# Performance work log

Hardware: AMD Instinct MI355X
Metric: run time of the kernel (lower is better)

The kernel has to match this reference:

```python
import jax, jax.numpy as jnp
import numpy as np

N_NODES = 100000


def _degrees(idx, n):
    d = jax.ops.segment_sum(jnp.ones(idx.shape[0], jnp.float32), idx, num_segments=n)
    return jnp.maximum(d, 1.0)  # DGL clamps zero degrees to 1


def graph_conv(src, dst, x, W, b, n):
    # DGL GraphConv with norm='both': out = D_in^{-1/2} A D_out^{-1/2} x W + b
    norm_src = _degrees(src, n) ** -0.5  # out-degree of source nodes
    norm_dst = _degrees(dst, n) ** -0.5  # in-degree of destination nodes
    xs = x * norm_src[:, None]
    msgs = xs[src]                                    # [E, d] gather
    agg = jax.ops.segment_sum(msgs, dst, num_segments=n)  # [N, d] scatter-add
    agg = agg * norm_dst[:, None]
    return agg @ W + b


def setup_inputs() -> dict:
    key = jax.random.key(0)
    k = jax.random.split(key, 7)
    E = 1600000
    in_f, h_f, out_f = 128, 128, 64
    return {
        "in_feat": jax.random.normal(k[0], (N_NODES, in_f), jnp.float32),
        "src": jax.random.randint(k[1], (E,), 0, N_NODES, jnp.int32),
        "dst": jax.random.randint(k[2], (E,), 0, N_NODES, jnp.int32),
        "W1": jax.random.normal(k[3], (in_f, h_f), jnp.float32) * (1.0 / np.sqrt(in_f)),
        "b1": jnp.zeros((h_f,), jnp.float32),
        "W2": jax.random.normal(k[4], (h_f, out_f), jnp.float32) * (1.0 / np.sqrt(h_f)),
        "b2": jnp.zeros((out_f,), jnp.float32),
    }


def reference(in_feat, src, dst, W1, b1, W2, b2):
    h = graph_conv(src, dst, in_feat, W1, b1, N_NODES)
    h = jax.nn.relu(h)
    h = graph_conv(src, dst, h, W2, b2, N_NODES)
    return h
```

## Files before the change

kernel.cpp:

```cpp
#include <hip/hip_runtime.h>

#define SLOT_CAP 64
#define NB_MAX 1024
#define CAP 2560

typedef __attribute__((ext_vector_type(8))) short bf16x8;
typedef __attribute__((ext_vector_type(4))) float f32x4;

__device__ __forceinline__ unsigned int bf16_rne(float f) {
    unsigned int u = __float_as_uint(f);
    return (u + 0x7FFFu + ((u >> 16) & 1u)) >> 16;
}
__device__ __forceinline__ unsigned int pack2(float a, float b) {
    return bf16_rne(a) | (bf16_rne(b) << 16);
}
__device__ __forceinline__ float bflo(unsigned int u) { return __uint_as_float(u << 16); }
__device__ __forceinline__ float bfhi(unsigned int u) { return __uint_as_float(u & 0xFFFF0000u); }
__device__ __forceinline__ float bf16val(unsigned int h) { return __uint_as_float(h << 16); }

__device__ __forceinline__ void gemm_tile(
    unsigned short* smem_us,
    const float* __restrict__ A,
    const unsigned short* __restrict__ wt_hi_g, const unsigned short* __restrict__ wt_lo_g,
    unsigned short* __restrict__ C, int M, int row0, int tid)
{
    unsigned short* As_hi = smem_us;
    unsigned short* As_lo = As_hi + 64 * 40;
    unsigned short* Ws_hi = As_lo + 64 * 40;
    unsigned short* Ws_lo = Ws_hi + 128 * 40;

    const int wv = tid >> 6;
    const int ln = tid & 63;
    const int fr = ln & 15;
    const int fk = ln >> 4;

    f32x4 acc[8];
#pragma unroll
    for (int t = 0; t < 8; t++) acc[t] = (f32x4){0.0f, 0.0f, 0.0f, 0.0f};

    const int sr = tid >> 2;
    const int sq = (tid & 3) * 8;

    for (int k0 = 0; k0 < 128; k0 += 32) {
        __syncthreads();
        {
            const int row = row0 + sr;
            float v0 = 0, v1 = 0, v2 = 0, v3 = 0, v4 = 0, v5 = 0, v6 = 0, v7 = 0;
            if (row < M) {
                const float4 p0 = *(const float4*)&A[(size_t)row * 128 + k0 + sq];
                const float4 p1 = *(const float4*)&A[(size_t)row * 128 + k0 + sq + 4];
                v0 = p0.x; v1 = p0.y; v2 = p0.z; v3 = p0.w;
                v4 = p1.x; v5 = p1.y; v6 = p1.z; v7 = p1.w;
            }
            unsigned int h0 = bf16_rne(v0), h1 = bf16_rne(v1), h2 = bf16_rne(v2), h3 = bf16_rne(v3);
            unsigned int h4 = bf16_rne(v4), h5 = bf16_rne(v5), h6 = bf16_rne(v6), h7 = bf16_rne(v7);
            uint4 hi, lo;
            hi.x = h0 | (h1 << 16); hi.y = h2 | (h3 << 16);
            hi.z = h4 | (h5 << 16); hi.w = h6 | (h7 << 16);
            lo.x = bf16_rne(v0 - bf16val(h0)) | (bf16_rne(v1 - bf16val(h1)) << 16);
            lo.y = bf16_rne(v2 - bf16val(h2)) | (bf16_rne(v3 - bf16val(h3)) << 16);
            lo.z = bf16_rne(v4 - bf16val(h4)) | (bf16_rne(v5 - bf16val(h5)) << 16);
            lo.w = bf16_rne(v6 - bf16val(h6)) | (bf16_rne(v7 - bf16val(h7)) << 16);
            *(uint4*)&As_hi[sr * 40 + sq] = hi;
            *(uint4*)&As_lo[sr * 40 + sq] = lo;
        }
#pragma unroll
        for (int j = 0; j < 8; j++) {
            int idx = tid + 256 * j;
            int c = idx >> 4, k2 = (idx & 15) * 2;
            *(unsigned int*)&Ws_hi[c * 40 + k2] = *(const unsigned int*)&wt_hi_g[c * 128 + k0 + k2];
            *(unsigned int*)&Ws_lo[c * 40 + k2] = *(const unsigned int*)&wt_lo_g[c * 128 + k0 + k2];
        }
        __syncthreads();

        bf16x8 ah = *(const bf16x8*)&As_hi[(16 * wv + fr) * 40 + fk * 8];
        bf16x8 al = *(const bf16x8*)&As_lo[(16 * wv + fr) * 40 + fk * 8];
#pragma unroll
        for (int t = 0; t < 8; t++) {
            bf16x8 bh = *(const bf16x8*)&Ws_hi[(16 * t + fr) * 40 + fk * 8];
            bf16x8 bl = *(const bf16x8*)&Ws_lo[(16 * t + fr) * 40 + fk * 8];
            acc[t] = __builtin_amdgcn_mfma_f32_16x16x32_bf16(ah, bh, acc[t], 0, 0, 0);
            acc[t] = __builtin_amdgcn_mfma_f32_16x16x32_bf16(al, bh, acc[t], 0, 0, 0);
            acc[t] = __builtin_amdgcn_mfma_f32_16x16x32_bf16(ah, bl, acc[t], 0, 0, 0);
        }
    }
#pragma unroll
    for (int t = 0; t < 8; t++) {
#pragma unroll
        for (int rg = 0; rg < 4; rg++) {
            int row = row0 + 16 * wv + fk * 4 + rg;
            if (row < M) C[(size_t)row * 128 + 16 * t + fr] = (unsigned short)bf16_rne(acc[t][rg]);
        }
    }
}

__global__ __launch_bounds__(256) void prep_w_kernel(
    const float* __restrict__ W1, unsigned short* __restrict__ wt_hi,
    unsigned short* __restrict__ wt_lo, int* __restrict__ cursor, int NB)
{
    if (blockIdx.x >= 64) {
        for (int i = (blockIdx.x - 64) * 256 + threadIdx.x; i < 2 * NB; i += 512)
            cursor[i] = 0;
        return;
    }
    const int idx = blockIdx.x * 256 + threadIdx.x;
    const int c = idx >> 7, k = idx & 127;
    float v = W1[k * 128 + c];
    unsigned int h = bf16_rne(v);
    wt_hi[idx] = (unsigned short)h;
    wt_lo[idx] = (unsigned short)bf16_rne(v - bf16val(h));
}

__global__ __launch_bounds__(256) void kb_kernel(
    const int* __restrict__ src, const int* __restrict__ dst,
    int* __restrict__ cursor,
    unsigned int* __restrict__ edge_shuf,
    unsigned char* __restrict__ src_shuf,
    int E, int NB, int EB,
    const float* __restrict__ A,
    const unsigned short* __restrict__ wt_hi_g, const unsigned short* __restrict__ wt_lo_g,
    unsigned short* __restrict__ C, int M)
{
    __shared__ __align__(16) char smem_raw[30720];
    const int tid = threadIdx.x;
    const int bid = blockIdx.x;

    if (bid >= EB) {
        int row0 = (bid - EB) * 64;
        if (row0 < M) gemm_tile((unsigned short*)smem_raw, A, wt_hi_g, wt_lo_g, C, M, row0, tid);
        return;
    }

    int* cntL = (int*)smem_raw;
    int* ofsL = cntL + 2 * NB_MAX;
    const int base = bid * 8192;
    for (int b = tid; b < 2 * NB; b += 256) cntL[b] = 0;
    __syncthreads();
#pragma unroll
    for (int it = 0; it < 8; it++) {
        const int i4 = base + (it * 256 + tid) * 4;
        if (i4 + 3 < E) {
            int4 s = *(const int4*)(src + i4);
            int4 d = *(const int4*)(dst + i4);
            atomicAdd(&cntL[d.x >> 7], 1); atomicAdd(&cntL[d.y >> 7], 1);
            atomicAdd(&cntL[d.z >> 7], 1); atomicAdd(&cntL[d.w >> 7], 1);
            atomicAdd(&cntL[NB + (s.x >> 7)], 1); atomicAdd(&cntL[NB + (s.y >> 7)], 1);
            atomicAdd(&cntL[NB + (s.z >> 7)], 1); atomicAdd(&cntL[NB + (s.w >> 7)], 1);
        } else {
            for (int i = i4; i < E && i < i4 + 4; i++) {
                atomicAdd(&cntL[dst[i] >> 7], 1);
                atomicAdd(&cntL[NB + (src[i] >> 7)], 1);
            }
        }
    }
    __syncthreads();
    for (int b = tid; b < 2 * NB; b += 256) {
        int c = cntL[b];
        ofsL[b] = c ? atomicAdd(&cursor[b], c) : 0;
    }
    __syncthreads();
#pragma unroll
    for (int it = 0; it < 8; it++) {
        const int i4 = base + (it * 256 + tid) * 4;
        if (i4 + 3 < E) {
            int4 s = *(const int4*)(src + i4);
            int4 d = *(const int4*)(dst + i4);
            { int bb = d.x >> 7; int p = atomicAdd(&ofsL[bb], 1); if (p < CAP) edge_shuf[(size_t)bb * CAP + p] = (unsigned)s.x | ((unsigned)(d.x & 127) << 17); }
            { int bb = d.y >> 7; int p = atomicAdd(&ofsL[bb], 1); if (p < CAP) edge_shuf[(size_t)bb * CAP + p] = (unsigned)s.y | ((unsigned)(d.y & 127) << 17); }
            { int bb = d.z >> 7; int p = atomicAdd(&ofsL[bb], 1); if (p < CAP) edge_shuf[(size_t)bb * CAP + p] = (unsigned)s.z | ((unsigned)(d.z & 127) << 17); }
            { int bb = d.w >> 7; int p = atomicAdd(&ofsL[bb], 1); if (p < CAP) edge_shuf[(size_t)bb * CAP + p] = (unsigned)s.w | ((unsigned)(d.w & 127) << 17); }
            { int bb = s.x >> 7; int q = atomicAdd(&ofsL[NB + bb], 1); if (q < CAP) src_shuf[(size_t)bb * CAP + q] = (unsigned char)(s.x & 127); }
            { int bb = s.y >> 7; int q = atomicAdd(&ofsL[NB + bb], 1); if (q < CAP) src_shuf[(size_t)bb * CAP + q] = (unsigned char)(s.y & 127); }
            { int bb = s.z >> 7; int q = atomicAdd(&ofsL[NB + bb], 1); if (q < CAP) src_shuf[(size_t)bb * CAP + q] = (unsigned char)(s.z & 127); }
            { int bb = s.w >> 7; int q = atomicAdd(&ofsL[NB + bb], 1); if (q < CAP) src_shuf[(size_t)bb * CAP + q] = (unsigned char)(s.w & 127); }
        } else {
            for (int i = i4; i < E && i < i4 + 4; i++) {
                int sv = src[i], dv = dst[i];
                int bb = dv >> 7; int p = atomicAdd(&ofsL[bb], 1);
                if (p < CAP) edge_shuf[(size_t)bb * CAP + p] = (unsigned)sv | ((unsigned)(dv & 127) << 17);
                int bs = sv >> 7; int q = atomicAdd(&ofsL[NB + bs], 1);
                if (q < CAP) src_shuf[(size_t)bs * CAP + q] = (unsigned char)(sv & 127);
            }
        }
    }
}

__global__ __launch_bounds__(256) void kc_src_kernel(
    const unsigned char* __restrict__ src_shuf, const int* __restrict__ cursor,
    int* __restrict__ cnt_src, int N, int NB)
{
    __shared__ int cntL[128];
    const int tid = threadIdx.x;
    const int b = blockIdx.x;
    if (tid < 128) cntL[tid] = 0;
    __syncthreads();
    const int start = b * CAP;
    const int len = min(cursor[NB + b], CAP);
    for (int i = start + tid; i < start + len; i += 256)
        atomicAdd(&cntL[src_shuf[i]], 1);
    __syncthreads();
    if (tid < 128) {
        int node = b * 128 + tid;
        if (node < N) cnt_src[node] = cntL[tid];
    }
}

#define ACC8(V_, S_) \
    acc[0] = fmaf(bflo((V_).x), (S_), acc[0]); acc[1] = fmaf(bfhi((V_).x), (S_), acc[1]); \
    acc[2] = fmaf(bflo((V_).y), (S_), acc[2]); acc[3] = fmaf(bfhi((V_).y), (S_), acc[3]); \
    acc[4] = fmaf(bflo((V_).z), (S_), acc[4]); acc[5] = fmaf(bfhi((V_).z), (S_), acc[5]); \
    acc[6] = fmaf(bflo((V_).w), (S_), acc[6]); acc[7] = fmaf(bfhi((V_).w), (S_), acc[7]);

#define SUM8(V_) \
    acc[0] += bflo((V_).x); acc[1] += bfhi((V_).x); \
    acc[2] += bflo((V_).y); acc[3] += bfhi((V_).y); \
    acc[4] += bflo((V_).z); acc[5] += bfhi((V_).z); \
    acc[6] += bflo((V_).w); acc[7] += bfhi((V_).w);

__global__ __launch_bounds__(256) void pg2_kernel(
    const int* __restrict__ cnt_src, const unsigned int* __restrict__ edge_shuf,
    const int* __restrict__ cursor,
    const unsigned int* __restrict__ msg,
    const float* __restrict__ W2, const float* __restrict__ b1,
    unsigned short* __restrict__ C, int N)
{
    __shared__ int cntL[32];
    __shared__ __align__(16) unsigned int slotsW[32 * SLOT_CAP];
    __shared__ unsigned int Agp[64][66];
    const int tid = threadIdx.x;
    const int hb = blockIdx.x;
    const int m0 = hb * 64;
    const int lane = tid & 15;
    const int b = hb >> 1;
    const int start = b * CAP;
    const int len = min(cursor[b], CAP);

#pragma unroll
    for (int half = 0; half < 2; half++) {
        if (tid < 32) cntL[tid] = 0;
        __syncthreads();
        const int dlo = (hb & 1) * 64 + half * 32;
        for (int i = start + tid; i < start + len; i += 256) {
            unsigned e = edge_shuf[i];
            int d = (int)(e >> 17) - dlo;
            if ((unsigned)d < 32u) {
                unsigned s = e & 0x1FFFFu;
                unsigned deg = (unsigned)min(cnt_src[s], 255);
                int r = atomicAdd(&cntL[d], 1);
                if (r < SLOT_CAP) slotsW[d * SLOT_CAP + r] = s | (deg << 17);
            }
        }
        __syncthreads();
#pragma unroll
        for (int p = 0; p < 2; p++) {
            const int nl32 = p * 16 + (tid >> 4);
            const int nl = half * 32 + nl32;
            const int node = m0 + nl;
            float acc[8];
#pragma unroll
            for (int k = 0; k < 8; k++) acc[k] = 0.0f;
            if (node < N) {
                const unsigned int* sl = &slotsW[nl32 * SLOT_CAP];
                const int cd = cntL[nl32];
                const int len2 = min(cd, SLOT_CAP);
                int j = 0;
                for (; j + 7 < len2; j += 8) {
                    uint4 e0 = *(const uint4*)(sl + j);
                    uint4 e1 = *(const uint4*)(sl + j + 4);
                    uint4 a0 = *(const uint4*)(msg + (size_t)(e0.x & 0x1FFFFu) * 64 + lane * 4);
                    uint4 a1 = *(const uint4*)(msg + (size_t)(e0.y & 0x1FFFFu) * 64 + lane * 4);
                    uint4 a2 = *(const uint4*)(msg + (size_t)(e0.z & 0x1FFFFu) * 64 + lane * 4);
                    uint4 a3 = *(const uint4*)(msg + (size_t)(e0.w & 0x1FFFFu) * 64 + lane * 4);
                    uint4 a4 = *(const uint4*)(msg + (size_t)(e1.x & 0x1FFFFu) * 64 + lane * 4);
                    uint4 a5 = *(const uint4*)(msg + (size_t)(e1.y & 0x1FFFFu) * 64 + lane * 4);
                    uint4 a6 = *(const uint4*)(msg + (size_t)(e1.z & 0x1FFFFu) * 64 + lane * 4);
                    uint4 a7 = *(const uint4*)(msg + (size_t)(e1.w & 0x1FFFFu) * 64 + lane * 4);
                    float w0 = rsqrtf((float)(e0.x >> 17));
                    float w1 = rsqrtf((float)(e0.y >> 17));
                    float w2 = rsqrtf((float)(e0.z >> 17));
                    float w3 = rsqrtf((float)(e0.w >> 17));
                    float w4 = rsqrtf((float)(e1.x >> 17));
                    float w5 = rsqrtf((float)(e1.y >> 17));
                    float w6 = rsqrtf((float)(e1.z >> 17));
                    float w7 = rsqrtf((float)(e1.w >> 17));
                    ACC8(a0, w0) ACC8(a1, w1) ACC8(a2, w2) ACC8(a3, w3)
                    ACC8(a4, w4) ACC8(a5, w5) ACC8(a6, w6) ACC8(a7, w7)
                }
                for (; j + 3 < len2; j += 4) {
                    uint4 e0 = *(const uint4*)(sl + j);
                    uint4 a0 = *(const uint4*)(msg + (size_t)(e0.x & 0x1FFFFu) * 64 + lane * 4);
                    uint4 a1 = *(const uint4*)(msg + (size_t)(e0.y & 0x1FFFFu) * 64 + lane * 4);
                    uint4 a2 = *(const uint4*)(msg + (size_t)(e0.z & 0x1FFFFu) * 64 + lane * 4);
                    uint4 a3 = *(const uint4*)(msg + (size_t)(e0.w & 0x1FFFFu) * 64 + lane * 4);
                    float w0 = rsqrtf((float)(e0.x >> 17));
                    float w1 = rsqrtf((float)(e0.y >> 17));
                    float w2 = rsqrtf((float)(e0.z >> 17));
                    float w3 = rsqrtf((float)(e0.w >> 17));
                    ACC8(a0, w0) ACC8(a1, w1) ACC8(a2, w2) ACC8(a3, w3)
                }
                for (; j < len2; j++) {
                    unsigned e = sl[j];
                    uint4 a0 = *(const uint4*)(msg + (size_t)(e & 0x1FFFFu) * 64 + lane * 4);
                    float w0 = rsqrtf((float)(e >> 17));
                    ACC8(a0, w0)
                }
                float nd = rsqrtf(fmaxf((float)cd, 1.0f));
                float ns = rsqrtf(fmaxf((float)cnt_src[node], 1.0f));
                float4 bA = *(const float4*)(b1 + lane * 8);
                float4 bB = *(const float4*)(b1 + lane * 8 + 4);
                acc[0] = fmaxf(fmaf(nd, acc[0], bA.x), 0.0f) * ns;
                acc[1] = fmaxf(fmaf(nd, acc[1], bA.y), 0.0f) * ns;
                acc[2] = fmaxf(fmaf(nd, acc[2], bA.z), 0.0f) * ns;
                acc[3] = fmaxf(fmaf(nd, acc[3], bA.w), 0.0f) * ns;
                acc[4] = fmaxf(fmaf(nd, acc[4], bB.x), 0.0f) * ns;
                acc[5] = fmaxf(fmaf(nd, acc[5], bB.y), 0.0f) * ns;
                acc[6] = fmaxf(fmaf(nd, acc[6], bB.z), 0.0f) * ns;
                acc[7] = fmaxf(fmaf(nd, acc[7], bB.w), 0.0f) * ns;
            }
            uint4 pk;
            pk.x = pack2(acc[0], acc[1]);
            pk.y = pack2(acc[2], acc[3]);
            pk.z = pack2(acc[4], acc[5]);
            pk.w = pack2(acc[6], acc[7]);
            *(uint4*)&Agp[nl][lane * 4] = pk;
        }
        __syncthreads();
    }

    float* Ws = (float*)slotsW;
    const int cx = tid & 15;
    const int rg = tid >> 4;
    float acc2[4][4];
#pragma unroll
    for (int r = 0; r < 4; r++)
#pragma unroll
        for (int c = 0; c < 4; c++) acc2[r][c] = 0.0f;

    for (int k0 = 0; k0 < 128; k0 += 32) {
#pragma unroll
        for (int jj = 0; jj < 8; jj++) {
            int idx = tid + 256 * jj;
            Ws[idx] = W2[k0 * 64 + idx];
        }
        __syncthreads();
#pragma unroll
        for (int kh = 0; kh < 16; kh++) {
            float4 wA = *(const float4*)&Ws[(2 * kh) * 64 + cx * 4];
            float4 wB = *(const float4*)&Ws[(2 * kh + 1) * 64 + cx * 4];
#pragma unroll
            for (int r = 0; r < 4; r++) {
                unsigned int u = Agp[rg * 4 + r][(k0 >> 1) + kh];
                float a0 = bflo(u), a1 = bfhi(u);
                acc2[r][0] = fmaf(a0, wA.x, acc2[r][0]);
                acc2[r][1] = fmaf(a0, wA.y, acc2[r][1]);
                acc2[r][2] = fmaf(a0, wA.z, acc2[r][2]);
                acc2[r][3] = fmaf(a0, wA.w, acc2[r][3]);
                acc2[r][0] = fmaf(a1, wB.x, acc2[r][0]);
                acc2[r][1] = fmaf(a1, wB.y, acc2[r][1]);
                acc2[r][2] = fmaf(a1, wB.z, acc2[r][2]);
                acc2[r][3] = fmaf(a1, wB.w, acc2[r][3]);
            }
        }
        __syncthreads();
    }
#pragma unroll
    for (int r = 0; r < 4; r++) {
        int row = m0 + rg * 4 + r;
        if (row < N) {
            uint2 p;
            p.x = pack2(acc2[r][0], acc2[r][1]);
            p.y = pack2(acc2[r][2], acc2[r][3]);
            *(uint2*)&C[(size_t)row * 64 + cx * 4] = p;
        }
    }
}

__global__ __launch_bounds__(256) void pull64_kernel(
    const unsigned int* __restrict__ edge_shuf, const int* __restrict__ cursor,
    const unsigned int* __restrict__ msg,
    const float* __restrict__ b2, float* __restrict__ out, int N)
{
    __shared__ int cntL[64];
    __shared__ __align__(16) unsigned int slotsL[64 * SLOT_CAP];
    const int tid = threadIdx.x;
    const int hb = blockIdx.x;
    const int m0 = hb * 64;

    if (tid < 64) cntL[tid] = 0;
    __syncthreads();
    {
        const int b = hb >> 1;
        const int dlo = (hb & 1) * 64;
        const int start = b * CAP;
        const int len = min(cursor[b], CAP);
        for (int i = start + tid; i < start + len; i += 256) {
            unsigned e = edge_shuf[i];
            int d = (int)(e >> 17) - dlo;
            if ((unsigned)d < 64u) {
                int r = atomicAdd(&cntL[d], 1);
                if (r < SLOT_CAP) slotsL[d * SLOT_CAP + r] = e & 0x1FFFFu;
            }
        }
    }
    __syncthreads();

    const int lane = tid & 7;
#pragma unroll
    for (int p = 0; p < 2; p++) {
        const int nl = p * 32 + (tid >> 3);
        const int node = m0 + nl;
        if (node >= N) continue;
        const unsigned int* sl = &slotsL[nl * SLOT_CAP];
        const int cd = cntL[nl];
        const int len = min(cd, SLOT_CAP);
        float acc[8];
#pragma unroll
        for (int k = 0; k < 8; k++) acc[k] = 0.0f;
        int j = 0;
        for (; j + 7 < len; j += 8) {
            uint4 e0 = *(const uint4*)(sl + j);
            uint4 e1 = *(const uint4*)(sl + j + 4);
            uint4 a0 = *(const uint4*)(msg + (size_t)e0.x * 32 + lane * 4);
            uint4 a1 = *(const uint4*)(msg + (size_t)e0.y * 32 + lane * 4);
            uint4 a2 = *(const uint4*)(msg + (size_t)e0.z * 32 + lane * 4);
            uint4 a3 = *(const uint4*)(msg + (size_t)e0.w * 32 + lane * 4);
            uint4 a4 = *(const uint4*)(msg + (size_t)e1.x * 32 + lane * 4);
            uint4 a5 = *(const uint4*)(msg + (size_t)e1.y * 32 + lane * 4);
            uint4 a6 = *(const uint4*)(msg + (size_t)e1.z * 32 + lane * 4);
            uint4 a7 = *(const uint4*)(msg + (size_t)e1.w * 32 + lane * 4);
            SUM8(a0) SUM8(a1) SUM8(a2) SUM8(a3) SUM8(a4) SUM8(a5) SUM8(a6) SUM8(a7)
        }
        for (; j + 3 < len; j += 4) {
            uint4 e0 = *(const uint4*)(sl + j);
            uint4 a0 = *(const uint4*)(msg + (size_t)e0.x * 32 + lane * 4);
            uint4 a1 = *(const uint4*)(msg + (size_t)e0.y * 32 + lane * 4);
            uint4 a2 = *(const uint4*)(msg + (size_t)e0.z * 32 + lane * 4);
            uint4 a3 = *(const uint4*)(msg + (size_t)e0.w * 32 + lane * 4);
            SUM8(a0) SUM8(a1) SUM8(a2) SUM8(a3)
        }
        for (; j < len; j++) {
            uint4 a0 = *(const uint4*)(msg + (size_t)sl[j] * 32 + lane * 4);
            SUM8(a0)
        }
        float nd = rsqrtf(fmaxf((float)cd, 1.0f));
        const float* bb = b2 + lane * 8;
        float4 bA = *(const float4*)(bb);
        float4 bB = *(const float4*)(bb + 4);
        float* o = out + (size_t)node * 64 + lane * 8;
        *(float4*)(o)     = make_float4(fmaf(acc[0], nd, bA.x), fmaf(acc[1], nd, bA.y),
                                        fmaf(acc[2], nd, bA.z), fmaf(acc[3], nd, bA.w));
        *(float4*)(o + 4) = make_float4(fmaf(acc[4], nd, bB.x), fmaf(acc[5], nd, bB.y),
                                        fmaf(acc[6], nd, bB.z), fmaf(acc[7], nd, bB.w));
    }
}

extern "C" void kernel_launch(void* const* d_in, const int* in_sizes, int n_in,
                              void* d_out, int out_size, void* d_ws, size_t ws_size,
                              hipStream_t stream) {
    const float* x   = (const float*)d_in[0];
    const int*   src = (const int*)d_in[1];
    const int*   dst = (const int*)d_in[2];
    const float* W1  = (const float*)d_in[3];
    const float* b1  = (const float*)d_in[4];
    const float* W2  = (const float*)d_in[5];
    const float* b2  = (const float*)d_in[6];
    float* out = (float*)d_out;

    const int E = in_sizes[1];
    const int N = in_sizes[0] / 128;
    const int NB = (N + 127) >> 7;

    int* iws = (int*)d_ws;
    int* cnt_src = iws;
    int* cursor  = cnt_src + N;
    unsigned int* edge_shuf = (unsigned int*)(cursor + 2 * NB);
    unsigned char* src_shuf = (unsigned char*)(edge_shuf + (size_t)NB * CAP);
    unsigned short* xw1 = (unsigned short*)(src_shuf + (((size_t)NB * CAP + 3) & ~(size_t)3));
    unsigned short* hw2 = xw1 + (size_t)N * 128;
    unsigned short* wt_hi = hw2 + (size_t)N * 64;
    unsigned short* wt_lo = wt_hi + 128 * 128;

    const int EB = (E + 8191) / 8192;
    const int GB = (N + 63) / 64;

    prep_w_kernel<<<66, 256, 0, stream>>>(W1, wt_hi, wt_lo, cursor, NB);

    kb_kernel<<<EB + GB, 256, 0, stream>>>(src, dst, cursor, edge_shuf, src_shuf,
                                           E, NB, EB, x, wt_hi, wt_lo, xw1, N);

    kc_src_kernel<<<NB, 256, 0, stream>>>(src_shuf, cursor, cnt_src, N, NB);

    pg2_kernel<<<(N + 63) / 64, 256, 0, stream>>>(
        cnt_src, edge_shuf, cursor, (const unsigned int*)xw1, W2, b1, hw2, N);

    pull64_kernel<<<(N + 63) / 64, 256, 0, stream>>>(
        edge_shuf, cursor, (const unsigned int*)hw2, b2, out, N);
}
```

Baseline: 316.8 us.

## Partition gather loops into source-index range passes for cache locality

Replaces the unrolled gather-accumulate loops in both pull kernels with a multi-pass loop. Each pass only loads messages whose source index falls in one range, 16K rows for the 128-wide bf16 layer and 32K rows for the 64-wide layer. The aim is for all concurrently running blocks to touch the same slice of the message table at once, so it stays resident in L2 or MALL cache. In exchange, the edge slot list is rescanned once per pass, the 8-way unrolling that gave memory-level parallelism is removed, and a data-dependent branch is added.

```diff
diff --git a/kernel.cpp b/kernel.cpp
--- a/kernel.cpp
+++ b/kernel.cpp
@@ -234,6 +234,7 @@
     const int b = hb >> 1;
     const int start = b * CAP;
     const int len = min(cursor[b], CAP);
+    const int NPASS = (N + 16383) >> 14;
 
 #pragma unroll
     for (int half = 0; half < 2; half++) {
@@ -263,46 +264,16 @@
                 const unsigned int* sl = &slotsW[nl32 * SLOT_CAP];
                 const int cd = cntL[nl32];
                 const int len2 = min(cd, SLOT_CAP);
-                int j = 0;
-                for (; j + 7 < len2; j += 8) {
-                    uint4 e0 = *(const uint4*)(sl + j);
-                    uint4 e1 = *(const uint4*)(sl + j + 4);
-                    uint4 a0 = *(const uint4*)(msg + (size_t)(e0.x & 0x1FFFFu) * 64 + lane * 4);
-                    uint4 a1 = *(const uint4*)(msg + (size_t)(e0.y & 0x1FFFFu) * 64 + lane * 4);
-                    uint4 a2 = *(const uint4*)(msg + (size_t)(e0.z & 0x1FFFFu) * 64 + lane * 4);
-                    uint4 a3 = *(const uint4*)(msg + (size_t)(e0.w & 0x1FFFFu) * 64 + lane * 4);
-                    uint4 a4 = *(const uint4*)(msg + (size_t)(e1.x & 0x1FFFFu) * 64 + lane * 4);
-                    uint4 a5 = *(const uint4*)(msg + (size_t)(e1.y & 0x1FFFFu) * 64 + lane * 4);
-                    uint4 a6 = *(const uint4*)(msg + (size_t)(e1.z & 0x1FFFFu) * 64 + lane * 4);
-                    uint4 a7 = *(const uint4*)(msg + (size_t)(e1.w & 0x1FFFFu) * 64 + lane * 4);
-                    float w0 = rsqrtf((float)(e0.x >> 17));
-                    float w1 = rsqrtf((float)(e0.y >> 17));
-                    float w2 = rsqrtf((float)(e0.z >> 17));
-                    float w3 = rsqrtf((float)(e0.w >> 17));
-                    float w4 = rsqrtf((float)(e1.x >> 17));
-                    float w5 = rsqrtf((float)(e1.y >> 17));
-                    float w6 = rsqrtf((float)(e1.z >> 17));
-                    float w7 = rsqrtf((float)(e1.w >> 17));
-                    ACC8(a0, w0) ACC8(a1, w1) ACC8(a2, w2) ACC8(a3, w3)
-                    ACC8(a4, w4) ACC8(a5, w5) ACC8(a6, w6) ACC8(a7, w7)
-                }
-                for (; j + 3 < len2; j += 4) {
-                    uint4 e0 = *(const uint4*)(sl + j);
-                    uint4 a0 = *(const uint4*)(msg + (size_t)(e0.x & 0x1FFFFu) * 64 + lane * 4);
-                    uint4 a1 = *(const uint4*)(msg + (size_t)(e0.y & 0x1FFFFu) * 64 + lane * 4);
-                    uint4 a2 = *(const uint4*)(msg + (size_t)(e0.z & 0x1FFFFu) * 64 + lane * 4);
-                    uint4 a3 = *(const uint4*)(msg + (size_t)(e0.w & 0x1FFFFu) * 64 + lane * 4);
-                    float w0 = rsqrtf((float)(e0.x >> 17));
-                    float w1 = rsqrtf((float)(e0.y >> 17));
-                    float w2 = rsqrtf((float)(e0.z >> 17));
-                    float w3 = rsqrtf((float)(e0.w >> 17));
-                    ACC8(a0, w0) ACC8(a1, w1) ACC8(a2, w2) ACC8(a3, w3)
-                }
-                for (; j < len2; j++) {
-                    unsigned e = sl[j];
-                    uint4 a0 = *(const uint4*)(msg + (size_t)(e & 0x1FFFFu) * 64 + lane * 4);
-                    float w0 = rsqrtf((float)(e >> 17));
-                    ACC8(a0, w0)
+                for (int pass = 0; pass < NPASS; pass++) {
+                    for (int j = 0; j < len2; j++) {
+                        unsigned e = sl[j];
+                        unsigned s = e & 0x1FFFFu;
+                        if ((int)(s >> 14) == pass) {
+                            uint4 a0 = *(const uint4*)(msg + (size_t)s * 64 + lane * 4);
+                            float w0 = rsqrtf((float)(e >> 17));
+                            ACC8(a0, w0)
+                        }
+                    }
                 }
                 float nd = rsqrtf(fmaxf((float)cd, 1.0f));
                 float ns = rsqrtf(fmaxf((float)cnt_src[node], 1.0f));
@@ -385,6 +356,7 @@
     const int tid = threadIdx.x;
     const int hb = blockIdx.x;
     const int m0 = hb * 64;
+    const int NPASS = (N + 32767) >> 15;
 
     if (tid < 64) cntL[tid] = 0;
     __syncthreads();
@@ -416,31 +388,14 @@
         float acc[8];
 #pragma unroll
         for (int k = 0; k < 8; k++) acc[k] = 0.0f;
-        int j = 0;
-        for (; j + 7 < len; j += 8) {
-            uint4 e0 = *(const uint4*)(sl + j);
-            uint4 e1 = *(const uint4*)(sl + j + 4);
-            uint4 a0 = *(const uint4*)(msg + (size_t)e0.x * 32 + lane * 4);
-            uint4 a1 = *(const uint4*)(msg + (size_t)e0.y * 32 + lane * 4);
-            uint4 a2 = *(const uint4*)(msg + (size_t)e0.z * 32 + lane * 4);
-            uint4 a3 = *(const uint4*)(msg + (size_t)e0.w * 32 + lane * 4);
-            uint4 a4 = *(const uint4*)(msg + (size_t)e1.x * 32 + lane * 4);
-            uint4 a5 = *(const uint4*)(msg + (size_t)e1.y * 32 + lane * 4);
-            uint4 a6 = *(const uint4*)(msg + (size_t)e1.z * 32 + lane * 4);
-            uint4 a7 = *(const uint4*)(msg + (size_t)e1.w * 32 + lane * 4);
-            SUM8(a0) SUM8(a1) SUM8(a2) SUM8(a3) SUM8(a4) SUM8(a5) SUM8(a6) SUM8(a7)
-        }
-        for (; j + 3 < len; j += 4) {
-            uint4 e0 = *(const uint4*)(sl + j);
-            uint4 a0 = *(const uint4*)(msg + (size_t)e0.x * 32 + lane * 4);
-            uint4 a1 = *(const uint4*)(msg + (size_t)e0.y * 32 + lane * 4);
-            uint4 a2 = *(const uint4*)(msg + (size_t)e0.z * 32 + lane * 4);
-            uint4 a3 = *(const uint4*)(msg + (size_t)e0.w * 32 + lane * 4);
-            SUM8(a0) SUM8(a1) SUM8(a2) SUM8(a3)
-        }
-        for (; j < len; j++) {
-            uint4 a0 = *(const uint4*)(msg + (size_t)sl[j] * 32 + lane * 4);
-            SUM8(a0)
+        for (int pass = 0; pass < NPASS; pass++) {
+            for (int j = 0; j < len; j++) {
+                unsigned s = sl[j];
+                if ((int)(s >> 15) == pass) {
+                    uint4 a0 = *(const uint4*)(msg + (size_t)s * 32 + lane * 4);
+                    SUM8(a0)
+                }
+            }
         }
         float nd = rsqrtf(fmaxf((float)cd, 1.0f));
         const float* bb = b2 + lane * 8;
```

Result: slower. 496.6 us (+56.8%).

## Fold W1 bf16 split into GEMM tiles and halve edges per binning block

Applied to the files above, without the earlier changes.

Removes the separate W1 preparation kernel. Each GEMM tile now reads W1 directly in fp32 and splits it into bf16 hi/lo parts while staging it into shared memory. The cursor reset becomes a hipMemsetAsync. The edge-binning blocks now process 4096 edges instead of 8192, which doubles the number of binning blocks for more parallelism. The trade-offs are redundant W1 conversion in every GEMM tile, strided fp32 W1 loads, and more global cursor atomics.

```diff
diff --git a/kernel.cpp b/kernel.cpp
--- a/kernel.cpp
+++ b/kernel.cpp
@@ -20,8 +20,7 @@
 
 __device__ __forceinline__ void gemm_tile(
     unsigned short* smem_us,
-    const float* __restrict__ A,
-    const unsigned short* __restrict__ wt_hi_g, const unsigned short* __restrict__ wt_lo_g,
+    const float* __restrict__ A, const float* __restrict__ W1,
     unsigned short* __restrict__ C, int M, int row0, int tid)
 {
     unsigned short* As_hi = smem_us;
@@ -67,9 +66,13 @@
 #pragma unroll
         for (int j = 0; j < 8; j++) {
             int idx = tid + 256 * j;
-            int c = idx >> 4, k2 = (idx & 15) * 2;
-            *(unsigned int*)&Ws_hi[c * 40 + k2] = *(const unsigned int*)&wt_hi_g[c * 128 + k0 + k2];
-            *(unsigned int*)&Ws_lo[c * 40 + k2] = *(const unsigned int*)&wt_lo_g[c * 128 + k0 + k2];
+            int c = idx >> 4, kp = (idx & 15) * 2;
+            float vA = W1[(size_t)(k0 + kp) * 128 + c];
+            float vB = W1[(size_t)(k0 + kp + 1) * 128 + c];
+            unsigned int hA = bf16_rne(vA), hB = bf16_rne(vB);
+            *(unsigned int*)&Ws_hi[c * 40 + kp] = hA | (hB << 16);
+            *(unsigned int*)&Ws_lo[c * 40 + kp] =
+                bf16_rne(vA - bf16val(hA)) | (bf16_rne(vB - bf16val(hB)) << 16);
         }
         __syncthreads();
 
@@ -94,31 +97,13 @@
     }
 }
 
-__global__ __launch_bounds__(256) void prep_w_kernel(
-    const float* __restrict__ W1, unsigned short* __restrict__ wt_hi,
-    unsigned short* __restrict__ wt_lo, int* __restrict__ cursor, int NB)
-{
-    if (blockIdx.x >= 64) {
-        for (int i = (blockIdx.x - 64) * 256 + threadIdx.x; i < 2 * NB; i += 512)
-            cursor[i] = 0;
-        return;
-    }
-    const int idx = blockIdx.x * 256 + threadIdx.x;
-    const int c = idx >> 7, k = idx & 127;
-    float v = W1[k * 128 + c];
-    unsigned int h = bf16_rne(v);
-    wt_hi[idx] = (unsigned short)h;
-    wt_lo[idx] = (unsigned short)bf16_rne(v - bf16val(h));
-}
-
 __global__ __launch_bounds__(256) void kb_kernel(
     const int* __restrict__ src, const int* __restrict__ dst,
     int* __restrict__ cursor,
     unsigned int* __restrict__ edge_shuf,
     unsigned char* __restrict__ src_shuf,
     int E, int NB, int EB,
-    const float* __restrict__ A,
-    const unsigned short* __restrict__ wt_hi_g, const unsigned short* __restrict__ wt_lo_g,
+    const float* __restrict__ A, const float* __restrict__ W1,
     unsigned short* __restrict__ C, int M)
 {
     __shared__ __align__(16) char smem_raw[30720];
@@ -127,17 +112,17 @@
 
     if (bid >= EB) {
         int row0 = (bid - EB) * 64;
-        if (row0 < M) gemm_tile((unsigned short*)smem_raw, A, wt_hi_g, wt_lo_g, C, M, row0, tid);
+        if (row0 < M) gemm_tile((unsigned short*)smem_raw, A, W1, C, M, row0, tid);
         return;
     }
 
     int* cntL = (int*)smem_raw;
     int* ofsL = cntL + 2 * NB_MAX;
-    const int base = bid * 8192;
+    const int base = bid * 4096;
     for (int b = tid; b < 2 * NB; b += 256) cntL[b] = 0;
     __syncthreads();
 #pragma unroll
-    for (int it = 0; it < 8; it++) {
+    for (int it = 0; it < 4; it++) {
         const int i4 = base + (it * 256 + tid) * 4;
         if (i4 + 3 < E) {
             int4 s = *(const int4*)(src + i4);
@@ -160,7 +145,7 @@
     }
     __syncthreads();
 #pragma unroll
-    for (int it = 0; it < 8; it++) {
+    for (int it = 0; it < 4; it++) {
         const int i4 = base + (it * 256 + tid) * 4;
         if (i4 + 3 < E) {
             int4 s = *(const int4*)(src + i4);
@@ -477,16 +462,14 @@
     unsigned char* src_shuf = (unsigned char*)(edge_shuf + (size_t)NB * CAP);
     unsigned short* xw1 = (unsigned short*)(src_shuf + (((size_t)NB * CAP + 3) & ~(size_t)3));
     unsigned short* hw2 = xw1 + (size_t)N * 128;
-    unsigned short* wt_hi = hw2 + (size_t)N * 64;
-    unsigned short* wt_lo = wt_hi + 128 * 128;
-
-    const int EB = (E + 8191) / 8192;
+
+    hipMemsetAsync(cursor, 0, 2 * (size_t)NB * sizeof(int), stream);
+
+    const int EB = (E + 4095) / 4096;
     const int GB = (N + 63) / 64;
 
-    prep_w_kernel<<<66, 256, 0, stream>>>(W1, wt_hi, wt_lo, cursor, NB);
-
     kb_kernel<<<EB + GB, 256, 0, stream>>>(src, dst, cursor, edge_shuf, src_shuf,
-                                           E, NB, EB, x, wt_hi, wt_lo, xw1, N);
+                                           E, NB, EB, x, W1, xw1, N);
 
     kc_src_kernel<<<NB, 256, 0, stream>>>(src_shuf, cursor, cnt_src, N, NB);
 
```

New measurement: 343.9 us. 1.09x slower.
